# Performance work log

Measured on AMD Instinct MI355X. Metric: run time of the kernel, lower is better.

Reference implementation:

```python
import jax, jax.numpy as jnp
import numpy as np

LENGTH = 320  # hard-coded in the layer
BIG = 1e5     # cap for 'no zero pixel in column' distances; BIG**2 = 1e10 -> exp() underflows to 0


def _edt_sq(zero):
    """Exact squared Euclidean distance transform.

    zero: [N, H, W] bool, True where the uint8-restored mask is 0 (seed pixels).
    Returns [N, H, W] float32 squared distance of every pixel to the nearest seed.
    Phase 1: 1D distance along H via associative scans (nearest seed above/below).
    Phase 2: exact lower envelope over W via a vectorized min-reduction:
             D2[n,i,j] = min_x ( (j-x)^2 + g2[n,i,x] ).
    """
    N, H, W = zero.shape
    ih = jnp.arange(H, dtype=jnp.float32)[None, :, None]            # [1,H,1]
    last = jax.lax.associative_scan(jnp.maximum,
                                    jnp.where(zero, ih, -BIG), axis=1)
    nxt = jax.lax.associative_scan(jnp.minimum,
                                   jnp.where(zero, ih, 2.0 * BIG), axis=1,
                                   reverse=True)
    g = jnp.minimum(jnp.minimum(ih - last, nxt - ih), BIG)           # [N,H,W] 1D dist
    g2 = g * g
    jw = jnp.arange(W, dtype=jnp.float32)
    off = (jw[:, None] - jw[None, :]) ** 2                           # [Wj, Wx]
    # [N,H,Wj,Wx] broadcast + min over source column x
    d2 = jnp.min(g2[:, :, None, :] + off[None, None], axis=-1)
    return d2


def _forward(inputs):
    B, H, W, _ = inputs.shape
    # uint8 cast: zero iff (1-x)*127.5 < 1  (matches tf.cast truncation)
    restored = ((1.0 - jax.lax.stop_gradient(inputs)) * 127.5).astype(jnp.uint8)
    zero = restored == 0                                             # [B,H,W,2]
    zm = jnp.moveaxis(zero, -1, 1).reshape(B * 2, H, W)              # fold channel into batch
    d2 = _edt_sq(zm).reshape(B, 2, H, W)
    sigmas = jnp.asarray([0.02, 0.08, 0.16], jnp.float32) * LENGTH   # [3]
    denom = 2.0 * sigmas * sigmas
    # exp(-d^2 / (2 sigma^2)) for each (channel, sigma); channel-major order like the loop
    clicks = jnp.exp(-d2[:, :, None] / denom[None, None, :, None, None])  # [B,2,3,H,W]
    return jnp.moveaxis(clicks.reshape(B, 6, H, W), 1, -1)          # [B,H,W,6]


def setup_inputs() -> dict:
    key = jax.random.key(0)
    inputs = jax.random.uniform(key, (4, 320, 320, 2), dtype=jnp.float32)
    return {"inputs": inputs}


def reference(inputs):
    return _forward(inputs)
```

## Files before the change

kernel.cpp:

```cpp
#include <hip/hip_runtime.h>

#define HH 320
#define WW 320
#define NIMG 8
#define BIGF 1.0e5f

#define TW  16
#define NCH 32
#define CH  10

__global__ __launch_bounds__(512) void edt_vert(const float* __restrict__ in,
                                                float* __restrict__ g2) {
    int wl = threadIdx.x;
    int ch = threadIdx.y;
    int b  = blockIdx.x / 20;
    int wt = blockIdx.x % 20;
    int w  = wt * TW + wl;
    int h0 = ch * CH;

    const float2* ip = (const float2*)in + (size_t)(b * HH + h0) * WW + w;
    float2 v[CH];
    #pragma unroll
    for (int k = 0; k < CH; ++k) v[k] = ip[(size_t)k * WW];

    unsigned m0 = 0, m1 = 0;
    #pragma unroll
    for (int k = 0; k < CH; ++k) {
        if ((1.0f - v[k].x) * 127.5f < 1.0f) m0 |= 1u << k;
        if ((1.0f - v[k].y) * 127.5f < 1.0f) m1 |= 1u << k;
    }

    __shared__ float sL[2][NCH][TW], sN[2][NCH][TW];
    sL[0][ch][wl] = m0 ? (float)(h0 + 31 - __clz((int)m0)) : -1.0e9f;
    sL[1][ch][wl] = m1 ? (float)(h0 + 31 - __clz((int)m1)) : -1.0e9f;
    sN[0][ch][wl] = m0 ? (float)(h0 + __ffs((int)m0) - 1)  :  1.0e9f;
    sN[1][ch][wl] = m1 ? (float)(h0 + __ffs((int)m1) - 1)  :  1.0e9f;
    __syncthreads();

    float L0 = -1.0e9f, L1 = -1.0e9f, N0 = 1.0e9f, N1 = 1.0e9f;
    for (int cc = 0; cc < NCH; ++cc) {
        float a0 = sL[0][cc][wl], a1 = sL[1][cc][wl];
        float b0 = sN[0][cc][wl], b1 = sN[1][cc][wl];
        if (cc < ch) { L0 = fmaxf(L0, a0); L1 = fmaxf(L1, a1); }
        if (cc > ch) { N0 = fminf(N0, b0); N1 = fminf(N1, b1); }
    }

    float gd0[CH], gd1[CH];
    float r0 = L0, r1 = L1;
    #pragma unroll
    for (int k = 0; k < CH; ++k) {
        float fh = (float)(h0 + k);
        if (m0 & (1u << k)) r0 = fh;
        if (m1 & (1u << k)) r1 = fh;
        gd0[k] = fh - r0;
        gd1[k] = fh - r1;
    }
    float* gp0 = g2 + ((size_t)(b * 2 + 0) * HH + h0) * WW + w;
    float* gp1 = g2 + ((size_t)(b * 2 + 1) * HH + h0) * WW + w;
    r0 = N0; r1 = N1;
    #pragma unroll
    for (int k = CH - 1; k >= 0; --k) {
        float fh = (float)(h0 + k);
        if (m0 & (1u << k)) r0 = fh;
        if (m1 & (1u << k)) r1 = fh;
        float g0 = fminf(fminf(gd0[k], r0 - fh), BIGF);
        float g1 = fminf(fminf(gd1[k], r1 - fh), BIGF);
        gp0[(size_t)k * WW] = g0 * g0;
        gp1[(size_t)k * WW] = g1 * g1;
    }
}

__global__ __launch_bounds__(256) void edt_horiz(const float* __restrict__ g2,
                                                 float* __restrict__ out) {
    int wv   = threadIdx.x >> 6;
    int lane = threadIdx.x & 63;
    int b  = blockIdx.x / 160;
    int hp = blockIdx.x % 160;
    int hh = wv >> 1;
    int c  = wv & 1;
    int row = (2 * b + c) * HH + (2 * hp + hh);

    __shared__ __align__(16) float sa[4][WW];
    __shared__ float scm[4][10];
    __shared__ float sd2[2][2][WW];

    const float* grow = g2 + (size_t)row * WW;
    #pragma unroll
    for (int m = 0; m < 5; ++m) {
        int x = lane + 64 * m;
        float g = grow[x];
        float fx = (float)x;
        sa[wv][x] = fmaf(fx, fx, g);
        float v = g;
        v = fminf(v, __shfl_xor(v, 1));
        v = fminf(v, __shfl_xor(v, 2));
        v = fminf(v, __shfl_xor(v, 4));
        v = fminf(v, __shfl_xor(v, 8));
        v = fminf(v, __shfl_xor(v, 16));
        if ((lane & 31) == 0) scm[wv][2 * m + (lane >> 5)] = v;
    }

    const float4* sv = (const float4*)sa[wv];
    float d2v[5], n2j[5];
    #pragma unroll
    for (int m = 0; m < 5; ++m) {
        d2v[m] = 3.4e38f;
        n2j[m] = -2.0f * (float)(lane + 64 * m);
    }

    auto scanChunk = [&](int m, int ck) {
        int q0 = ck * 8;
        #pragma unroll
        for (int u = 0; u < 8; u += 2) {
            float4 f0 = sv[q0 + u];
            float4 f1 = sv[q0 + u + 1];
            float xb = (float)(ck * 32 + 4 * u);
            float av[8] = {f0.x, f0.y, f0.z, f0.w, f1.x, f1.y, f1.z, f1.w};
            #pragma unroll
            for (int k = 0; k < 8; k += 2) {
                float t0 = fmaf(n2j[m], xb + (float)k,       av[k]);
                float t1 = fmaf(n2j[m], xb + (float)(k + 1), av[k + 1]);
                d2v[m] = fminf(d2v[m], fminf(t0, t1));
            }
        }
    };

    #pragma unroll
    for (int m = 0; m < 5; ++m) { scanChunk(m, 2 * m); scanChunk(m, 2 * m + 1); }

    for (int m = 0; m < 5; ++m) {
        float fj  = (float)(lane + 64 * m);
        float fj2 = fj * fj;
        bool goL = (m > 0), goR = (m < 4);
        for (int r = 1; r < 10 && (goL || goR); ++r) {
            int cl = 2 * m - r, cr = 2 * m + 1 + r;
            if (goL) {
                if (cl < 0) goL = false;
                else {
                    float thr = d2v[m] + fj2;
                    float gap = fj - (float)(32 * cl + 31);
                    float bb = gap * gap;
                    if (!__any(bb < thr)) goL = false;
                    else if (__any(bb + scm[wv][cl] < thr)) scanChunk(m, cl);
                }
            }
            if (goR) {
                if (cr > 9) goR = false;
                else {
                    float thr = d2v[m] + fj2;
                    float gap = (float)(32 * cr) - fj;
                    float bb = gap * gap;
                    if (!__any(bb < thr)) goR = false;
                    else if (__any(bb + scm[wv][cr] < thr)) scanChunk(m, cr);
                }
            }
        }
    }

    #pragma unroll
    for (int m = 0; m < 5; ++m) {
        float fj = (float)(lane + 64 * m);
        sd2[hh][c][lane + 64 * m] = fmaf(fj, fj, d2v[m]);
    }
    __syncthreads();

    float* obase = out + (size_t)(b * HH + 2 * hp) * WW * 6;
    for (int q = threadIdx.x; q < 960; q += 256) {
        int D = 4 * q;
        int hh2 = D / 1920;
        int rr = D - 1920 * hh2;
        float vals[4];
        #pragma unroll
        for (int e = 0; e < 4; ++e) {
            int idx = rr + e;
            int jj = idx / 6;
            int cs = idx - 6 * jj;
            int c2 = (cs >= 3) ? 1 : 0;
            int s  = cs - 3 * c2;
            float dd = sd2[hh2][c2][jj];
            float co = (s == 0) ? (1.0f / 81.92f)
                     : (s == 1) ? (1.0f / 1310.72f)
                                : (1.0f / 5242.88f);
            vals[e] = __expf(-dd * co);
        }
        float4 o = {vals[0], vals[1], vals[2], vals[3]};
        *(float4*)(obase + D) = o;
    }
}

extern "C" void kernel_launch(void* const* d_in, const int* in_sizes, int n_in,
                              void* d_out, int out_size, void* d_ws, size_t ws_size,
                              hipStream_t stream) {
    const float* in = (const float*)d_in[0];
    float* out = (float*)d_out;
    float* g2 = (float*)d_ws;

    edt_vert<<<4 * 20, dim3(TW, NCH), 0, stream>>>(in, g2);
    edt_horiz<<<4 * 160, 256, 0, stream>>>(g2, out);
}
```

Measured before the change: 86.28 us.

## Replace pruned chunk search with full brute-force min over all columns

Removes the per-chunk minimum precomputation and the warp-vote pruned expansion of neighbouring chunks in the horizontal pass. Every lane now scans all 320 source columns for all five of its output columns, double-buffering float4 loads from shared memory. This drops divergent control flow, shuffles and __any votes in exchange for doing the full O(W^2) arithmetic, which the pruning previously avoided. With random inputs most pixels have nearby seeds, so pruning was likely skipping much of the work.

```diff
diff --git a/kernel.cpp b/kernel.cpp
--- a/kernel.cpp
+++ b/kernel.cpp
@@ -81,23 +81,14 @@
     int row = (2 * b + c) * HH + (2 * hp + hh);
 
     __shared__ __align__(16) float sa[4][WW];
-    __shared__ float scm[4][10];
     __shared__ float sd2[2][2][WW];
 
     const float* grow = g2 + (size_t)row * WW;
     #pragma unroll
     for (int m = 0; m < 5; ++m) {
         int x = lane + 64 * m;
-        float g = grow[x];
         float fx = (float)x;
-        sa[wv][x] = fmaf(fx, fx, g);
-        float v = g;
-        v = fminf(v, __shfl_xor(v, 1));
-        v = fminf(v, __shfl_xor(v, 2));
-        v = fminf(v, __shfl_xor(v, 4));
-        v = fminf(v, __shfl_xor(v, 8));
-        v = fminf(v, __shfl_xor(v, 16));
-        if ((lane & 31) == 0) scm[wv][2 * m + (lane >> 5)] = v;
+        sa[wv][x] = fmaf(fx, fx, grow[x]);
     }
 
     const float4* sv = (const float4*)sa[wv];
@@ -108,53 +99,30 @@
         n2j[m] = -2.0f * (float)(lane + 64 * m);
     }
 
-    auto scanChunk = [&](int m, int ck) {
-        int q0 = ck * 8;
+    float4 cur[8], nxt[8];
+    #pragma unroll
+    for (int q = 0; q < 8; ++q) cur[q] = sv[q];
+    #pragma unroll
+    for (int t = 0; t < 10; ++t) {
+        if (t < 9) {
+            #pragma unroll
+            for (int q = 0; q < 8; ++q) nxt[q] = sv[8 * (t + 1) + q];
+        }
         #pragma unroll
-        for (int u = 0; u < 8; u += 2) {
-            float4 f0 = sv[q0 + u];
-            float4 f1 = sv[q0 + u + 1];
-            float xb = (float)(ck * 32 + 4 * u);
-            float av[8] = {f0.x, f0.y, f0.z, f0.w, f1.x, f1.y, f1.z, f1.w};
+        for (int q = 0; q < 8; ++q) {
+            float a0 = cur[q].x, a1 = cur[q].y, a2 = cur[q].z, a3 = cur[q].w;
+            float x0 = (float)(32 * t + 4 * q);
             #pragma unroll
-            for (int k = 0; k < 8; k += 2) {
-                float t0 = fmaf(n2j[m], xb + (float)k,       av[k]);
-                float t1 = fmaf(n2j[m], xb + (float)(k + 1), av[k + 1]);
-                d2v[m] = fminf(d2v[m], fminf(t0, t1));
+            for (int m = 0; m < 5; ++m) {
+                float t0 = fmaf(n2j[m], x0,        a0);
+                float t1 = fmaf(n2j[m], x0 + 1.0f, a1);
+                float t2 = fmaf(n2j[m], x0 + 2.0f, a2);
+                float t3 = fmaf(n2j[m], x0 + 3.0f, a3);
+                d2v[m] = fminf(fminf(d2v[m], fminf(t0, t1)), fminf(t2, t3));
             }
         }
-    };
-
-    #pragma unroll
-    for (int m = 0; m < 5; ++m) { scanChunk(m, 2 * m); scanChunk(m, 2 * m + 1); }
-
-    for (int m = 0; m < 5; ++m) {
-        float fj  = (float)(lane + 64 * m);
-        float fj2 = fj * fj;
-        bool goL = (m > 0), goR = (m < 4);
-        for (int r = 1; r < 10 && (goL || goR); ++r) {
-            int cl = 2 * m - r, cr = 2 * m + 1 + r;
-            if (goL) {
-                if (cl < 0) goL = false;
-                else {
-                    float thr = d2v[m] + fj2;
-                    float gap = fj - (float)(32 * cl + 31);
-                    float bb = gap * gap;
-                    if (!__any(bb < thr)) goL = false;
-                    else if (__any(bb + scm[wv][cl] < thr)) scanChunk(m, cl);
-                }
-            }
-            if (goR) {
-                if (cr > 9) goR = false;
-                else {
-                    float thr = d2v[m] + fj2;
-                    float gap = (float)(32 * cr) - fj;
-                    float bb = gap * gap;
-                    if (!__any(bb < thr)) goR = false;
-                    else if (__any(bb + scm[wv][cr] < thr)) scanChunk(m, cr);
-                }
-            }
-        }
+        #pragma unroll
+        for (int q = 0; q < 8; ++q) cur[q] = nxt[q];
     }
 
     #pragma unroll
```

After: 74.11 us, median of 2. 1.16x faster.
